# Kernel optimization log

Hardware: AMD Instinct MI355X
Metric: run time of the kernel (lower is better)

Reference implementation:

```python
import jax, jax.numpy as jnp
import numpy as np

N = 50000      # nodes
E = 800000     # edges
F_IN = 256     # num_n_feature
EMB = 128      # emb_size
GF = 32        # num_g_feature
G = 256        # graphs in batch
NEG_SLOPE = 0.2


def setup_inputs() -> dict:
    key = jax.random.key(0)
    ks = jax.random.split(key, 20)
    p = lambda i, shape: (jax.random.normal(ks[i], shape, jnp.float32) * 0.05)
    return {
        "x": jax.random.normal(ks[0], (N, F_IN), jnp.float32),
        "edges_idx": jax.random.randint(ks[1], (2, E), 0, N, dtype=jnp.int32),
        "batch_idx": jnp.sort(jax.random.randint(ks[2], (N,), 0, G, dtype=jnp.int32)),
        "g_features": jax.random.normal(ks[3], (G, GF), jnp.float32),
        # GATConv 1
        "W1": p(4, (F_IN, EMB)), "a1_src": p(5, (EMB,)), "a1_dst": p(6, (EMB,)), "b1": p(7, (EMB,)),
        # GATConv 2
        "W2": p(8, (EMB, EMB)), "a2_src": p(9, (EMB,)), "a2_dst": p(10, (EMB,)), "b2": p(11, (EMB,)),
        # lin_g
        "Wg": p(12, (GF, EMB)), "bg": p(13, (EMB,)),
        # out head: Linear(3*emb, 2)
        "Wo": p(14, (3 * EMB, 2)), "bo": p(15, (2,)),
    }


def gat_conv(x, src, dst, W, a_src, a_dst, b, n):
    """PyG GATConv, heads=1, with self-loops; attention dropout omitted (eval)."""
    h = x @ W                                  # [N, emb]
    loop = jnp.arange(n, dtype=src.dtype)
    src = jnp.concatenate([src, loop])         # add self loops
    dst = jnp.concatenate([dst, loop])
    e = jax.nn.leaky_relu((h @ a_src)[src] + (h @ a_dst)[dst], NEG_SLOPE)  # [E+N]
    # segment softmax over destination nodes
    m = jax.lax.stop_gradient(jax.ops.segment_max(e, dst, num_segments=n))
    m = jnp.where(jnp.isfinite(m), m, 0.0)
    p = jnp.exp(e - m[dst])
    den = jax.ops.segment_sum(p, dst, num_segments=n)
    alpha = p / den[dst]
    out = jax.ops.segment_sum(alpha[:, None] * h[src], dst, num_segments=n)
    return out + b


def reference(x, edges_idx, batch_idx, g_features,
              W1, a1_src, a1_dst, b1, W2, a2_src, a2_dst, b2,
              Wg, bg, Wo, bo):
    src, dst = edges_idx[0], edges_idx[1]
    h = gat_conv(x, src, dst, W1, a1_src, a1_dst, b1, N)
    h = gat_conv(h, src, dst, W2, a2_src, a2_dst, b2, N)
    # global mean / max pooling per graph
    counts = jax.ops.segment_sum(jnp.ones((N,), h.dtype), batch_idx, num_segments=G)
    mean = jax.ops.segment_sum(h, batch_idx, num_segments=G) / jnp.maximum(counts, 1.0)[:, None]
    mx = jax.ops.segment_max(h, batch_idx, num_segments=G)
    mx = jnp.where(jnp.isfinite(mx), mx, 0.0)
    g_ft = g_features @ Wg + bg
    flat = jnp.concatenate([mean, mx, g_ft], axis=1)   # [G, 3*emb]
    return jax.nn.log_softmax(flat @ Wo + bo, axis=-1)  # [G, 2]
```

## Files before the change

### kernel.cpp

```cpp
#include <hip/hip_runtime.h>
#include <hip/hip_bf16.h>

#define N_NODES 50000
#define N_EDGES 800000
#define FIN 256
#define EMB 128
#define NGRAPH 256
#define TOT_E (N_EDGES + N_NODES)
#define NP 98
#define RBLK 196

typedef __bf16 bf16;
typedef __attribute__((ext_vector_type(8))) __bf16 bf16x8;
typedef __attribute__((ext_vector_type(4))) __bf16 bf16x4;
typedef __attribute__((ext_vector_type(2))) __bf16 bf16x2;
typedef __attribute__((ext_vector_type(4))) float f32x4;
typedef __attribute__((ext_vector_type(4))) int i32x4;

__global__ void transpose2_kernel(const float* __restrict__ W1, bf16* __restrict__ WT1,
                                  const float* __restrict__ W2, bf16* __restrict__ WT2) {
    int t = blockIdx.x * 256 + threadIdx.x;
    if (t < FIN * EMB) {
        int c = t / FIN, r = t - c * FIN;
        WT1[t] = (bf16)W1[r * EMB + c];
    } else if (t < FIN * EMB + EMB * EMB) {
        int u = t - FIN * EMB;
        int c = u / EMB, r = u - c * EMB;
        WT2[u] = (bf16)W2[r * EMB + c];
    }
}


__global__ __launch_bounds__(256)
void hist_part_kernel(const int* __restrict__ e_dst, int* __restrict__ mat) {
    __shared__ int lh[NP];
    int t = threadIdx.x;
    for (int k = t; k < NP; k += 256) lh[k] = 0;
    __syncthreads();
    const int NQ = N_EDGES / 4;
    int base = blockIdx.x * 1024;
#pragma unroll
    for (int j = 0; j < 4; ++j) {
        int i = base + j * 256 + t;
        if (i < NQ) {
            i32x4 d4 = *(const i32x4*)(e_dst + 4 * i);
#pragma unroll
            for (int k = 0; k < 4; ++k) atomicAdd(&lh[d4[k] >> 9], 1);
        }
    }
    __syncthreads();
    for (int k = t; k < NP; k += 256) mat[k * RBLK + blockIdx.x] = lh[k];
}

__global__ __launch_bounds__(256)
void rowscan_kernel(int* __restrict__ mat, int* __restrict__ rowsum) {
    __shared__ int lds[256];
    int p = blockIdx.x, t = threadIdx.x;
    int v = (t < RBLK) ? mat[p * RBLK + t] : 0;
    lds[t] = v;
    __syncthreads();
    for (int d = 1; d < 256; d <<= 1) {
        int u = (t >= d) ? lds[t - d] : 0;
        __syncthreads();
        lds[t] += u;
        __syncthreads();
    }
    if (t < RBLK) mat[p * RBLK + t] = lds[t] - v;
    if (t == 255) rowsum[p] = lds[255];
}

__global__ __launch_bounds__(128)
void partbase_kernel(const int* __restrict__ rowsum, int* __restrict__ poff) {
    __shared__ int lds[128];
    int t = threadIdx.x;
    int v = (t < NP) ? rowsum[t] : 0;
    lds[t] = v;
    __syncthreads();
    for (int d = 1; d < 128; d <<= 1) {
        int u = (t >= d) ? lds[t - d] : 0;
        __syncthreads();
        lds[t] += u;
        __syncthreads();
    }
    if (t < NP) poff[t] = lds[t] - v;
    if (t == 0) poff[NP] = N_EDGES;
}

__global__ __launch_bounds__(256)
void radix_scatter_kernel(const int* __restrict__ e_src, const int* __restrict__ e_dst,
                          const int* __restrict__ mat, const int* __restrict__ poff,
                          unsigned* __restrict__ pairs) {
    __shared__ int cur[NP];
    int t = threadIdx.x;
    for (int k = t; k < NP; k += 256) cur[k] = poff[k] + mat[k * RBLK + blockIdx.x];
    __syncthreads();
    const int NQ = N_EDGES / 4;
    int base = blockIdx.x * 1024;
#pragma unroll
    for (int j = 0; j < 4; ++j) {
        int i = base + j * 256 + t;
        if (i < NQ) {
            i32x4 d4 = *(const i32x4*)(e_dst + 4 * i);
            i32x4 s4 = *(const i32x4*)(e_src + 4 * i);
#pragma unroll
            for (int k = 0; k < 4; ++k) {
                int d = d4[k];
                int pos = atomicAdd(&cur[d >> 9], 1);
                pairs[pos] = ((unsigned)d << 16) | (unsigned)s4[k];
            }
        }
    }
}

__global__ __launch_bounds__(1024)
void part_build_kernel(const int* __restrict__ poff, const unsigned* __restrict__ pairs,
                       int* __restrict__ offsets, int* __restrict__ sorted) {
    int p = blockIdx.x, t = threadIdx.x;
    int nbase = p * 512;
    int valid = N_NODES - nbase;
    valid = valid > 512 ? 512 : valid;
    __shared__ int cnt[512], sc[512];
    if (t < 512) cnt[t] = (t < valid) ? 1 : 0;
    __syncthreads();
    int p0 = poff[p], p1 = poff[p + 1];
    for (int i = p0 + t; i < p1; i += 1024)
        atomicAdd(&cnt[(pairs[i] >> 16) & 511], 1);
    __syncthreads();
    int v = (t < 512) ? cnt[t] : 0;
    if (t < 512) sc[t] = v;
    __syncthreads();
    for (int d = 1; d < 512; d <<= 1) {
        int u = (t < 512 && t >= d) ? sc[t - d] : 0;
        __syncthreads();
        if (t < 512) sc[t] += u;
        __syncthreads();
    }
    int base = p0 + nbase;
    if (t < valid) {
        int off = base + (sc[t] - v);
        offsets[nbase + t] = off;
        sorted[off] = nbase + t;
        cnt[t] = off + 1;
    }
    if (p == 0 && t == 0) offsets[N_NODES] = TOT_E;
    __syncthreads();
    for (int i = p0 + t; i < p1; i += 1024) {
        unsigned pr = pairs[i];
        int pos = atomicAdd(&cnt[(pr >> 16) & 511], 1);
        sorted[pos] = (int)(pr & 0xFFFFu);
    }
}

template<int K, typename AT>
__global__ __launch_bounds__(256)
void gemm_kernel(const AT* __restrict__ A, const bf16* __restrict__ WT,
                 bf16* __restrict__ C, int M,
                 const float* __restrict__ a_src, const float* __restrict__ a_dst,
                 float* __restrict__ s_src, float* __restrict__ s_dst) {
    __shared__ __align__(16) bf16 As[32][64];
    __shared__ __align__(16) bf16 Bs[128][64];
    __shared__ float sbuf[2][32];
    int tid = threadIdx.x;
    int wave = tid >> 6, lane = tid & 63;
    int rowHalf = wave & 1, colHalf = wave >> 1;
    int m0 = blockIdx.x * 32;

    f32x4 acc[4];
#pragma unroll
    for (int i = 0; i < 4; ++i) acc[i] = (f32x4){0.f, 0.f, 0.f, 0.f};

    for (int k0 = 0; k0 < K; k0 += 64) {
        if constexpr (sizeof(AT) == 4) {
#pragma unroll
            for (int it = 0; it < 2; ++it) {
                int task = tid + it * 256;
                int row = task >> 4, seg4 = task & 15;
                int gr = m0 + row;
                float4 f = make_float4(0.f, 0.f, 0.f, 0.f);
                if (gr < M) f = *(const float4*)((const float*)A + (size_t)gr * K + k0 + seg4 * 4);
                bf16x4 b4 = (bf16x4){(bf16)f.x, (bf16)f.y, (bf16)f.z, (bf16)f.w};
                int slot = seg4 >> 1, half8 = seg4 & 1;
                int ss = slot ^ (row & 7);
                *(bf16x4*)(&As[row][ss * 8 + half8 * 4]) = b4;
            }
        } else {
            int row = tid >> 3, slot = tid & 7;
            int gr = m0 + row;
            uint4 v = make_uint4(0u, 0u, 0u, 0u);
            if (gr < M) v = *(const uint4*)((const bf16*)A + (size_t)gr * K + k0 + slot * 8);
            int ss = slot ^ (row & 7);
            *(uint4*)(&As[row][ss * 8]) = v;
        }
#pragma unroll
        for (int it = 0; it < 4; ++it) {
            int task = tid + it * 256;
            int col = task >> 3, slot = task & 7;
            uint4 v = *(const uint4*)(WT + (size_t)col * K + k0 + slot * 8);
            int ss = slot ^ (col & 7);
            *(uint4*)(&Bs[col][ss * 8]) = v;
        }
        __syncthreads();
        int tr = rowHalf * 16 + (lane & 15);
        int kseg = lane >> 4;
        bf16x8 af0 = *(const bf16x8*)(&As[tr][((kseg) ^ (tr & 7)) * 8]);
        bf16x8 af1 = *(const bf16x8*)(&As[tr][((4 + kseg) ^ (tr & 7)) * 8]);
#pragma unroll
        for (int n = 0; n < 4; ++n) {
            int c = colHalf * 64 + n * 16 + (lane & 15);
            bf16x8 b0 = *(const bf16x8*)(&Bs[c][((kseg) ^ (c & 7)) * 8]);
            bf16x8 b1 = *(const bf16x8*)(&Bs[c][((4 + kseg) ^ (c & 7)) * 8]);
            acc[n] = __builtin_amdgcn_mfma_f32_16x16x32_bf16(af0, b0, acc[n], 0, 0, 0);
            acc[n] = __builtin_amdgcn_mfma_f32_16x16x32_bf16(af1, b1, acc[n], 0, 0, 0);
        }
        __syncthreads();
    }
    int rbase = m0 + rowHalf * 16 + ((lane >> 4) << 2);
    int cb = lane & 15;
#pragma unroll
    for (int n = 0; n < 4; ++n) {
        int col = colHalf * 64 + n * 16 + cb;
#pragma unroll
        for (int rr = 0; rr < 4; ++rr) {
            int row = rbase + rr;
            if (row < M) C[(size_t)row * 128 + col] = (bf16)acc[n][rr];
        }
    }
    if (tid < 64) sbuf[tid >> 5][tid & 31] = 0.f;
    __syncthreads();
    float a_s[4], a_d[4];
#pragma unroll
    for (int n = 0; n < 4; ++n) {
        a_s[n] = a_src[colHalf * 64 + n * 16 + cb];
        a_d[n] = a_dst[colHalf * 64 + n * 16 + cb];
    }
#pragma unroll
    for (int rr = 0; rr < 4; ++rr) {
        float ps = 0.f, pd = 0.f;
#pragma unroll
        for (int n = 0; n < 4; ++n) {
            ps += acc[n][rr] * a_s[n];
            pd += acc[n][rr] * a_d[n];
        }
#pragma unroll
        for (int mk = 8; mk >= 1; mk >>= 1) {
            ps += __shfl_xor(ps, mk);
            pd += __shfl_xor(pd, mk);
        }
        if (cb == 0) {
            int tr16 = rowHalf * 16 + (lane >> 4) * 4 + rr;
            atomicAdd(&sbuf[0][tr16], ps);
            atomicAdd(&sbuf[1][tr16], pd);
        }
    }
    __syncthreads();
    if (tid < 32 && m0 + tid < M) {
        s_src[m0 + tid] = sbuf[0][tid];
        s_dst[m0 + tid] = sbuf[1][tid];
    }
}

template<typename OUT_T>
__global__ __launch_bounds__(256)
void agg_kernel(const int* __restrict__ offsets, const int* __restrict__ sorted_src,
                const float* __restrict__ s_src, const float* __restrict__ s_dst,
                const bf16* __restrict__ h, const float* __restrict__ bias,
                OUT_T* __restrict__ out) {
    int tid = threadIdx.x;
    int wave = tid >> 6, lane = tid & 63;
    int gl = lane & 15;
    int gbase = lane & 48;
    int d = blockIdx.x * 16 + wave * 4 + (lane >> 4);
    if (d >= N_NODES) return;
    int r0 = offsets[d];
    int deg = offsets[d + 1] - r0;
    float sd = s_dst[d];

    int sv0 = 0, sv1 = 0;
    float ev0 = -INFINITY, ev1 = -INFINITY;
    if (gl < deg) {
        sv0 = sorted_src[r0 + gl];
        float e = s_src[sv0] + sd;
        ev0 = (e > 0.f) ? e : 0.2f * e;
    }
    if (16 + gl < deg) {
        sv1 = sorted_src[r0 + 16 + gl];
        float e = s_src[sv1] + sd;
        ev1 = (e > 0.f) ? e : 0.2f * e;
    }
    float m = fmaxf(ev0, ev1);
    for (int i = 32 + gl; i < deg; i += 16) {
        int s = sorted_src[r0 + i];
        float e = s_src[s] + sd;
        e = (e > 0.f) ? e : 0.2f * e;
        m = fmaxf(m, e);
    }
#pragma unroll
    for (int mk = 8; mk >= 1; mk >>= 1) m = fmaxf(m, __shfl_xor(m, mk));

    float pv0 = (gl < deg) ? __expf(ev0 - m) : 0.f;
    float pv1 = (16 + gl < deg) ? __expf(ev1 - m) : 0.f;
    float den = pv0 + pv1;
    for (int i = 32 + gl; i < deg; i += 16) {
        int s = sorted_src[r0 + i];
        float e = s_src[s] + sd;
        e = (e > 0.f) ? e : 0.2f * e;
        den += __expf(e - m);
    }
#pragma unroll
    for (int mk = 8; mk >= 1; mk >>= 1) den += __shfl_xor(den, mk);

    float acc[8];
#pragma unroll
    for (int k = 0; k < 8; ++k) acc[k] = 0.f;

    int jm = (deg < 32) ? deg : 32;
#pragma unroll 8
    for (int j = 0; j < jm; ++j) {
        int src_lane = gbase + (j & 15);
        int s = __shfl((j < 16) ? sv0 : sv1, src_lane);
        float p = __shfl((j < 16) ? pv0 : pv1, src_lane);
        bf16x8 hv = *(const bf16x8*)(h + (size_t)s * 128 + gl * 8);
#pragma unroll
        for (int k = 0; k < 8; ++k) acc[k] += p * (float)hv[k];
    }
    for (int i = 32; i < deg; ++i) {
        int s = sorted_src[r0 + i];
        float e = s_src[s] + sd;
        e = (e > 0.f) ? e : 0.2f * e;
        float p = __expf(e - m);
        bf16x8 hv = *(const bf16x8*)(h + (size_t)s * 128 + gl * 8);
#pragma unroll
        for (int k = 0; k < 8; ++k) acc[k] += p * (float)hv[k];
    }

    float inv = 1.f / den;
    float4 bv0 = *(const float4*)(bias + gl * 8);
    float4 bv1 = *(const float4*)(bias + gl * 8 + 4);
    float o[8] = {acc[0] * inv + bv0.x, acc[1] * inv + bv0.y,
                  acc[2] * inv + bv0.z, acc[3] * inv + bv0.w,
                  acc[4] * inv + bv1.x, acc[5] * inv + bv1.y,
                  acc[6] * inv + bv1.z, acc[7] * inv + bv1.w};
    if constexpr (sizeof(OUT_T) == 2) {
        bf16x8 ov;
#pragma unroll
        for (int k = 0; k < 8; ++k) ov[k] = (bf16)o[k];
        *(bf16x8*)((bf16*)out + (size_t)d * 128 + gl * 8) = ov;
    } else {
        float* op = (float*)out + (size_t)d * 128 + gl * 8;
        *(float4*)op       = (float4){o[0], o[1], o[2], o[3]};
        *(float4*)(op + 4) = (float4){o[4], o[5], o[6], o[7]};
    }
}

__global__ __launch_bounds__(256)
void pool_kernel(const bf16* __restrict__ out2, const int* __restrict__ batch_idx,
                 float* __restrict__ mean, float* __restrict__ mx) {
    int g = blockIdx.x;
    int j = threadIdx.x & 127;
    int grp = threadIdx.x >> 7;
    int lo = 0, hi = N_NODES;
    while (lo < hi) { int mid = (lo + hi) >> 1; if (batch_idx[mid] < g) lo = mid + 1; else hi = mid; }
    int start = lo;
    hi = N_NODES;
    while (lo < hi) { int mid = (lo + hi) >> 1; if (batch_idx[mid] < g + 1) lo = mid + 1; else hi = mid; }
    int end = lo;

    float s = 0.f, mmax = -INFINITY;
    for (int r = start + grp; r < end; r += 2) {
        float v = (float)out2[(size_t)r * 128 + j];
        s += v;
        mmax = fmaxf(mmax, v);
    }
    __shared__ float ls[2][128], lm[2][128];
    ls[grp][j] = s; lm[grp][j] = mmax;
    __syncthreads();
    if (grp == 0) {
        int cnt = end - start;
        float sum = ls[0][j] + ls[1][j];
        float mv = fmaxf(lm[0][j], lm[1][j]);
        mean[g * 128 + j] = sum / fmaxf((float)cnt, 1.f);
        mx[g * 128 + j] = (cnt > 0) ? mv : 0.f;
    }
}

__global__ __launch_bounds__(128)
void head_kernel(const float* __restrict__ mean, const float* __restrict__ mx,
                 const float* __restrict__ gfeat, const float* __restrict__ Wg,
                 const float* __restrict__ bg, const float* __restrict__ Wo,
                 const float* __restrict__ bo, float* __restrict__ out) {
    int g = blockIdx.x;
    int j = threadIdx.x;
    float gft = bg[j];
#pragma unroll
    for (int k = 0; k < 32; ++k)
        gft += gfeat[g * 32 + k] * Wg[k * 128 + j];
    float mj = mean[g * 128 + j], xj = mx[g * 128 + j];
    float p0 = mj * Wo[j * 2 + 0] + xj * Wo[(128 + j) * 2 + 0] + gft * Wo[(256 + j) * 2 + 0];
    float p1 = mj * Wo[j * 2 + 1] + xj * Wo[(128 + j) * 2 + 1] + gft * Wo[(256 + j) * 2 + 1];
#pragma unroll
    for (int m = 32; m >= 1; m >>= 1) { p0 += __shfl_xor(p0, m); p1 += __shfl_xor(p1, m); }
    __shared__ float l0s[2], l1s[2];
    int wv = j >> 6;
    if ((j & 63) == 0) { l0s[wv] = p0; l1s[wv] = p1; }
    __syncthreads();
    if (j == 0) {
        float l0 = l0s[0] + l0s[1] + bo[0];
        float l1 = l1s[0] + l1s[1] + bo[1];
        float mm = fmaxf(l0, l1);
        float lse = mm + logf(__expf(l0 - mm) + __expf(l1 - mm));
        out[g * 2 + 0] = l0 - lse;
        out[g * 2 + 1] = l1 - lse;
    }
}

extern "C" void kernel_launch(void* const* d_in, const int* in_sizes, int n_in,
                              void* d_out, int out_size, void* d_ws, size_t ws_size,
                              hipStream_t stream) {
    const float* x     = (const float*)d_in[0];
    const int*   edges = (const int*)d_in[1];
    const int*   batch = (const int*)d_in[2];
    const float* gfeat = (const float*)d_in[3];
    const float* W1    = (const float*)d_in[4];
    const float* a1s   = (const float*)d_in[5];
    const float* a1d   = (const float*)d_in[6];
    const float* b1    = (const float*)d_in[7];
    const float* W2    = (const float*)d_in[8];
    const float* a2s   = (const float*)d_in[9];
    const float* a2d   = (const float*)d_in[10];
    const float* b2    = (const float*)d_in[11];
    const float* Wg    = (const float*)d_in[12];
    const float* bg    = (const float*)d_in[13];
    const float* Wo    = (const float*)d_in[14];
    const float* bo    = (const float*)d_in[15];

    char* ws = (char*)d_ws;
    bf16*     WT1       = (bf16*)(ws + 0);
    bf16*     WT2       = (bf16*)(ws + 65536);
    float*    s_src     = (float*)(ws + 98304);
    float*    s_dst     = (float*)(ws + 299008);
    int*      mat       = (int*)(ws + 700672);
    int*      rowsum    = (int*)(ws + 777536);
    int*      poff      = (int*)(ws + 777984);
    int*      offsets   = (int*)(ws + 778432);
    int*      sorted    = (int*)(ws + 979136);
    bf16*     h         = (bf16*)(ws + 4502528);
    bf16*     out1      = (bf16*)(ws + 17302528);
    bf16*     out2      = (bf16*)(ws + 30102528);
    unsigned* pairs     = (unsigned*)(ws + 43002528);
    float*    pmean     = (float*)(ws + 55702528);
    float*    pmax      = (float*)(ws + 55833600);

    const int* e_src = edges;
    const int* e_dst = edges + N_EDGES;

    transpose2_kernel<<<(FIN * EMB + EMB * EMB + 255) / 256, 256, 0, stream>>>(W1, WT1, W2, WT2);

    hist_part_kernel<<<RBLK, 256, 0, stream>>>(e_dst, mat);
    rowscan_kernel<<<NP, 256, 0, stream>>>(mat, rowsum);
    partbase_kernel<<<1, 128, 0, stream>>>(rowsum, poff);
    radix_scatter_kernel<<<RBLK, 256, 0, stream>>>(e_src, e_dst, mat, poff, pairs);
    part_build_kernel<<<NP, 1024, 0, stream>>>(poff, pairs, offsets, sorted);

    int gemm_blocks = (N_NODES + 31) / 32;
    int agg_blocks = (N_NODES + 15) / 16;

    gemm_kernel<FIN, float><<<gemm_blocks, 256, 0, stream>>>(x, WT1, h, N_NODES,
                                                             a1s, a1d, s_src, s_dst);
    agg_kernel<bf16><<<agg_blocks, 256, 0, stream>>>(offsets, sorted, s_src, s_dst, h, b1, out1);

    gemm_kernel<EMB, bf16><<<gemm_blocks, 256, 0, stream>>>(out1, WT2, h, N_NODES,
                                                            a2s, a2d, s_src, s_dst);
    agg_kernel<bf16><<<agg_blocks, 256, 0, stream>>>(offsets, sorted, s_src, s_dst, h, b2, out2);

    pool_kernel<<<NGRAPH, 256, 0, stream>>>(out2, batch, pmean, pmax);
    head_kernel<<<NGRAPH, 128, 0, stream>>>(pmean, pmax, gfeat, Wg, bg, Wo, bo, (float*)d_out);
}
```

Baseline: 175.5 us.

## Fuse pooling into second aggregation with atomics and merge setup kernels

Merges the weight transpose, edge histogram and pooling-buffer zeroing into one setup kernel. Removes the partition-base kernel by recomputing the small prefix scan inside the scatter and build kernels. Fuses global mean/max pooling into the second aggregation kernel using float atomicAdd and an order-preserving unsigned atomicMax, dropping the pool kernel and the out2 buffer. This cuts launch count and a full pass over node features, but adds heavy atomic contention since nodes of the same graph are contiguous.

```diff
diff --git a/kernel.cpp b/kernel.cpp
--- a/kernel.cpp
+++ b/kernel.cpp
@@ -13,43 +13,49 @@
 typedef __bf16 bf16;
 typedef __attribute__((ext_vector_type(8))) __bf16 bf16x8;
 typedef __attribute__((ext_vector_type(4))) __bf16 bf16x4;
-typedef __attribute__((ext_vector_type(2))) __bf16 bf16x2;
 typedef __attribute__((ext_vector_type(4))) float f32x4;
 typedef __attribute__((ext_vector_type(4))) int i32x4;
 
-__global__ void transpose2_kernel(const float* __restrict__ W1, bf16* __restrict__ WT1,
-                                  const float* __restrict__ W2, bf16* __restrict__ WT2) {
-    int t = blockIdx.x * 256 + threadIdx.x;
-    if (t < FIN * EMB) {
-        int c = t / FIN, r = t - c * FIN;
-        WT1[t] = (bf16)W1[r * EMB + c];
-    } else if (t < FIN * EMB + EMB * EMB) {
-        int u = t - FIN * EMB;
-        int c = u / EMB, r = u - c * EMB;
-        WT2[u] = (bf16)W2[r * EMB + c];
-    }
-}
-
-
 __global__ __launch_bounds__(256)
-void hist_part_kernel(const int* __restrict__ e_dst, int* __restrict__ mat) {
+void setup_kernel(const int* __restrict__ e_dst, int* __restrict__ mat,
+                  const float* __restrict__ W1, bf16* __restrict__ WT1,
+                  const float* __restrict__ W2, bf16* __restrict__ WT2,
+                  float* __restrict__ pmean, unsigned* __restrict__ pmaxu) {
     __shared__ int lh[NP];
-    int t = threadIdx.x;
-    for (int k = t; k < NP; k += 256) lh[k] = 0;
-    __syncthreads();
-    const int NQ = N_EDGES / 4;
-    int base = blockIdx.x * 1024;
-#pragma unroll
-    for (int j = 0; j < 4; ++j) {
-        int i = base + j * 256 + t;
-        if (i < NQ) {
-            i32x4 d4 = *(const i32x4*)(e_dst + 4 * i);
-#pragma unroll
-            for (int k = 0; k < 4; ++k) atomicAdd(&lh[d4[k] >> 9], 1);
-        }
-    }
-    __syncthreads();
-    for (int k = t; k < NP; k += 256) mat[k * RBLK + blockIdx.x] = lh[k];
+    int b = blockIdx.x, t = threadIdx.x;
+    if (b < RBLK) {
+        for (int k = t; k < NP; k += 256) lh[k] = 0;
+        __syncthreads();
+        const int NQ = N_EDGES / 4;
+        int base = b * 1024;
+#pragma unroll
+        for (int j = 0; j < 4; ++j) {
+            int i = base + j * 256 + t;
+            if (i < NQ) {
+                i32x4 d4 = *(const i32x4*)(e_dst + 4 * i);
+#pragma unroll
+                for (int k = 0; k < 4; ++k) atomicAdd(&lh[d4[k] >> 9], 1);
+            }
+        }
+        __syncthreads();
+        for (int k = t; k < NP; k += 256) mat[k * RBLK + b] = lh[k];
+    } else if (b < RBLK + 192) {
+        int u = (b - RBLK) * 256 + t;
+        if (u < FIN * EMB) {
+            int c = u / FIN, r = u - c * FIN;
+            WT1[u] = (bf16)W1[r * EMB + c];
+        } else {
+            int v = u - FIN * EMB;
+            int c = v / EMB, r = v - c * EMB;
+            WT2[v] = (bf16)W2[r * EMB + c];
+        }
+    } else {
+        int u = (b - RBLK - 192) * 256 + t;
+        for (int i = u; i < NGRAPH * EMB; i += 4096) {
+            pmean[i] = 0.f;
+            pmaxu[i] = 0u;
+        }
+    }
 }
 
 __global__ __launch_bounds__(256)
@@ -69,30 +75,22 @@
     if (t == 255) rowsum[p] = lds[255];
 }
 
-__global__ __launch_bounds__(128)
-void partbase_kernel(const int* __restrict__ rowsum, int* __restrict__ poff) {
-    __shared__ int lds[128];
-    int t = threadIdx.x;
-    int v = (t < NP) ? rowsum[t] : 0;
-    lds[t] = v;
-    __syncthreads();
-    for (int d = 1; d < 128; d <<= 1) {
-        int u = (t >= d) ? lds[t - d] : 0;
-        __syncthreads();
-        lds[t] += u;
-        __syncthreads();
-    }
-    if (t < NP) poff[t] = lds[t] - v;
-    if (t == 0) poff[NP] = N_EDGES;
-}
-
 __global__ __launch_bounds__(256)
 void radix_scatter_kernel(const int* __restrict__ e_src, const int* __restrict__ e_dst,
-                          const int* __restrict__ mat, const int* __restrict__ poff,
+                          const int* __restrict__ mat, const int* __restrict__ rowsum,
                           unsigned* __restrict__ pairs) {
-    __shared__ int cur[NP];
+    __shared__ int ps[128], cur[NP];
     int t = threadIdx.x;
-    for (int k = t; k < NP; k += 256) cur[k] = poff[k] + mat[k * RBLK + blockIdx.x];
+    int rv = 0;
+    if (t < 128) { rv = (t < NP) ? rowsum[t] : 0; ps[t] = rv; }
+    __syncthreads();
+    for (int d = 1; d < 128; d <<= 1) {
+        int u = (t < 128 && t >= d) ? ps[t - d] : 0;
+        __syncthreads();
+        if (t < 128) ps[t] += u;
+        __syncthreads();
+    }
+    if (t < NP) cur[t] = (ps[t] - rv) + mat[t * RBLK + blockIdx.x];
     __syncthreads();
     const int NQ = N_EDGES / 4;
     int base = blockIdx.x * 1024;
@@ -113,16 +111,35 @@
 }
 
 __global__ __launch_bounds__(1024)
-void part_build_kernel(const int* __restrict__ poff, const unsigned* __restrict__ pairs,
+void part_build_kernel(const int* __restrict__ rowsum, const unsigned* __restrict__ pairs,
                        int* __restrict__ offsets, int* __restrict__ sorted) {
     int p = blockIdx.x, t = threadIdx.x;
+    __shared__ int ps[128];
+    __shared__ int sp0, sp1;
+    if (t < 128) {
+        int rv = (t < NP) ? rowsum[t] : 0;
+        ps[t] = rv;
+    }
+    __syncthreads();
+    for (int d = 1; d < 128; d <<= 1) {
+        int u = (t < 128 && t >= d) ? ps[t - d] : 0;
+        __syncthreads();
+        if (t < 128) ps[t] += u;
+        __syncthreads();
+    }
+    if (t == 0) {
+        int excl = ps[p] - rowsum[p];
+        sp0 = excl;
+        sp1 = excl + rowsum[p];
+    }
+    __syncthreads();
+    int p0 = sp0, p1 = sp1;
     int nbase = p * 512;
     int valid = N_NODES - nbase;
     valid = valid > 512 ? 512 : valid;
     __shared__ int cnt[512], sc[512];
     if (t < 512) cnt[t] = (t < valid) ? 1 : 0;
     __syncthreads();
-    int p0 = poff[p], p1 = poff[p + 1];
     for (int i = p0 + t; i < p1; i += 1024)
         atomicAdd(&cnt[(pairs[i] >> 16) & 511], 1);
     __syncthreads();
@@ -259,12 +276,13 @@
     }
 }
 
-template<typename OUT_T>
+template<bool POOL>
 __global__ __launch_bounds__(256)
 void agg_kernel(const int* __restrict__ offsets, const int* __restrict__ sorted_src,
                 const float* __restrict__ s_src, const float* __restrict__ s_dst,
                 const bf16* __restrict__ h, const float* __restrict__ bias,
-                OUT_T* __restrict__ out) {
+                bf16* __restrict__ out, const int* __restrict__ batch,
+                float* __restrict__ pmean, unsigned* __restrict__ pmaxu) {
     int tid = threadIdx.x;
     int wave = tid >> 6, lane = tid & 63;
     int gl = lane & 15;
@@ -340,61 +358,49 @@
                   acc[2] * inv + bv0.z, acc[3] * inv + bv0.w,
                   acc[4] * inv + bv1.x, acc[5] * inv + bv1.y,
                   acc[6] * inv + bv1.z, acc[7] * inv + bv1.w};
-    if constexpr (sizeof(OUT_T) == 2) {
+    if constexpr (POOL) {
+        int g = batch[d];
+#pragma unroll
+        for (int k = 0; k < 8; ++k) {
+            atomicAdd(&pmean[g * 128 + gl * 8 + k], o[k]);
+            unsigned bts = __float_as_uint(o[k]);
+            unsigned mu = (bts & 0x80000000u) ? ~bts : (bts | 0x80000000u);
+            atomicMax(&pmaxu[g * 128 + gl * 8 + k], mu);
+        }
+    } else {
         bf16x8 ov;
 #pragma unroll
         for (int k = 0; k < 8; ++k) ov[k] = (bf16)o[k];
-        *(bf16x8*)((bf16*)out + (size_t)d * 128 + gl * 8) = ov;
-    } else {
-        float* op = (float*)out + (size_t)d * 128 + gl * 8;
-        *(float4*)op       = (float4){o[0], o[1], o[2], o[3]};
-        *(float4*)(op + 4) = (float4){o[4], o[5], o[6], o[7]};
-    }
-}
-
-__global__ __launch_bounds__(256)
-void pool_kernel(const bf16* __restrict__ out2, const int* __restrict__ batch_idx,
-                 float* __restrict__ mean, float* __restrict__ mx) {
+        *(bf16x8*)(out + (size_t)d * 128 + gl * 8) = ov;
+    }
+}
+
+__global__ __launch_bounds__(128)
+void head_kernel(const float* __restrict__ pmean, const unsigned* __restrict__ pmaxu,
+                 const int* __restrict__ batch_idx,
+                 const float* __restrict__ gfeat, const float* __restrict__ Wg,
+                 const float* __restrict__ bg, const float* __restrict__ Wo,
+                 const float* __restrict__ bo, float* __restrict__ out) {
     int g = blockIdx.x;
-    int j = threadIdx.x & 127;
-    int grp = threadIdx.x >> 7;
+    int j = threadIdx.x;
     int lo = 0, hi = N_NODES;
     while (lo < hi) { int mid = (lo + hi) >> 1; if (batch_idx[mid] < g) lo = mid + 1; else hi = mid; }
     int start = lo;
     hi = N_NODES;
     while (lo < hi) { int mid = (lo + hi) >> 1; if (batch_idx[mid] < g + 1) lo = mid + 1; else hi = mid; }
-    int end = lo;
-
-    float s = 0.f, mmax = -INFINITY;
-    for (int r = start + grp; r < end; r += 2) {
-        float v = (float)out2[(size_t)r * 128 + j];
-        s += v;
-        mmax = fmaxf(mmax, v);
-    }
-    __shared__ float ls[2][128], lm[2][128];
-    ls[grp][j] = s; lm[grp][j] = mmax;
-    __syncthreads();
-    if (grp == 0) {
-        int cnt = end - start;
-        float sum = ls[0][j] + ls[1][j];
-        float mv = fmaxf(lm[0][j], lm[1][j]);
-        mean[g * 128 + j] = sum / fmaxf((float)cnt, 1.f);
-        mx[g * 128 + j] = (cnt > 0) ? mv : 0.f;
-    }
-}
-
-__global__ __launch_bounds__(128)
-void head_kernel(const float* __restrict__ mean, const float* __restrict__ mx,
-                 const float* __restrict__ gfeat, const float* __restrict__ Wg,
-                 const float* __restrict__ bg, const float* __restrict__ Wo,
-                 const float* __restrict__ bo, float* __restrict__ out) {
-    int g = blockIdx.x;
-    int j = threadIdx.x;
+    int cnt = lo - start;
+
+    float mj = pmean[g * 128 + j] / fmaxf((float)cnt, 1.f);
+    float xj = 0.f;
+    if (cnt > 0) {
+        unsigned mu = pmaxu[g * 128 + j];
+        unsigned bts = (mu & 0x80000000u) ? (mu ^ 0x80000000u) : ~mu;
+        xj = __uint_as_float(bts);
+    }
     float gft = bg[j];
 #pragma unroll
     for (int k = 0; k < 32; ++k)
         gft += gfeat[g * 32 + k] * Wg[k * 128 + j];
-    float mj = mean[g * 128 + j], xj = mx[g * 128 + j];
     float p0 = mj * Wo[j * 2 + 0] + xj * Wo[(128 + j) * 2 + 0] + gft * Wo[(256 + j) * 2 + 0];
     float p1 = mj * Wo[j * 2 + 1] + xj * Wo[(128 + j) * 2 + 1] + gft * Wo[(256 + j) * 2 + 1];
 #pragma unroll
@@ -440,38 +446,36 @@
     float*    s_dst     = (float*)(ws + 299008);
     int*      mat       = (int*)(ws + 700672);
     int*      rowsum    = (int*)(ws + 777536);
-    int*      poff      = (int*)(ws + 777984);
     int*      offsets   = (int*)(ws + 778432);
     int*      sorted    = (int*)(ws + 979136);
     bf16*     h         = (bf16*)(ws + 4502528);
     bf16*     out1      = (bf16*)(ws + 17302528);
-    bf16*     out2      = (bf16*)(ws + 30102528);
     unsigned* pairs     = (unsigned*)(ws + 43002528);
     float*    pmean     = (float*)(ws + 55702528);
-    float*    pmax      = (float*)(ws + 55833600);
+    unsigned* pmaxu     = (unsigned*)(ws + 55833600);
 
     const int* e_src = edges;
     const int* e_dst = edges + N_EDGES;
 
-    transpose2_kernel<<<(FIN * EMB + EMB * EMB + 255) / 256, 256, 0, stream>>>(W1, WT1, W2, WT2);
-
-    hist_part_kernel<<<RBLK, 256, 0, stream>>>(e_dst, mat);
+    setup_kernel<<<RBLK + 192 + 16, 256, 0, stream>>>(e_dst, mat, W1, WT1, W2, WT2,
+                                                      pmean, pmaxu);
     rowscan_kernel<<<NP, 256, 0, stream>>>(mat, rowsum);
-    partbase_kernel<<<1, 128, 0, stream>>>(rowsum, poff);
-    radix_scatter_kernel<<<RBLK, 256, 0, stream>>>(e_src, e_dst, mat, poff, pairs);
-    part_build_kernel<<<NP, 1024, 0, stream>>>(poff, pairs, offsets, sorted);
+    radix_scatter_kernel<<<RBLK, 256, 0, stream>>>(e_src, e_dst, mat, rowsum, pairs);
+    part_build_kernel<<<NP, 1024, 0, stream>>>(rowsum, pairs, offsets, sorted);
 
     int gemm_blocks = (N_NODES + 31) / 32;
     int agg_blocks = (N_NODES + 15) / 16;
 
     gemm_kernel<FIN, float><<<gemm_blocks, 256, 0, stream>>>(x, WT1, h, N_NODES,
                                                              a1s, a1d, s_src, s_dst);
-    agg_kernel<bf16><<<agg_blocks, 256, 0, stream>>>(offsets, sorted, s_src, s_dst, h, b1, out1);
+    agg_kernel<false><<<agg_blocks, 256, 0, stream>>>(offsets, sorted, s_src, s_dst,
+                                                      h, b1, out1, batch, pmean, pmaxu);
 
     gemm_kernel<EMB, bf16><<<gemm_blocks, 256, 0, stream>>>(out1, WT2, h, N_NODES,
                                                             a2s, a2d, s_src, s_dst);
-    agg_kernel<bf16><<<agg_blocks, 256, 0, stream>>>(offsets, sorted, s_src, s_dst, h, b2, out2);
-
-    pool_kernel<<<NGRAPH, 256, 0, stream>>>(out2, batch, pmean, pmax);
-    head_kernel<<<NGRAPH, 128, 0, stream>>>(pmean, pmax, gfeat, Wg, bg, Wo, bo, (float*)d_out);
-}
+    agg_kernel<true><<<agg_blocks, 256, 0, stream>>>(offsets, sorted, s_src, s_dst,
+                                                     h, b2, nullptr, batch, pmean, pmaxu);
+
+    head_kernel<<<NGRAPH, 128, 0, stream>>>(pmean, pmaxu, batch, gfeat, Wg, bg, Wo, bo,
+                                            (float*)d_out);
+}
```

Measured after the change: 525.7 us. 3x slower.
